# Performance work log

Measured on AMD Instinct MI355X. Metric: run time of the kernel, lower is better.

The kernel has to match this reference:

```python
import jax, jax.numpy as jnp
import numpy as np

N = 200000
E = 5000000


def _gcn_norm(edge_index, num_nodes):
    # add self-loops and compute symmetric normalization (PyG GCNConv default)
    loop = jnp.arange(num_nodes, dtype=edge_index.dtype)
    src = jnp.concatenate([edge_index[0], loop])
    dst = jnp.concatenate([edge_index[1], loop])
    ones = jnp.ones(dst.shape[0], dtype=jnp.float32)
    deg = jax.ops.segment_sum(ones, dst, num_segments=num_nodes)
    dis = jnp.where(deg > 0, jax.lax.rsqrt(deg), 0.0)
    norm = dis[src] * dis[dst]  # [E+N]
    return src, dst, norm


def _gcn_layer(x, src, dst, norm, W, b, num_nodes):
    xl = x @ W  # [N, out] dense linear (no bias, PyG default)
    msg = xl[src] * norm[:, None]  # gather + scale
    agg = jax.ops.segment_sum(msg, dst, num_segments=num_nodes)  # scatter-add
    return agg + b


def setup_inputs() -> dict:
    key = jax.random.key(0)
    ks = jax.random.split(key, 10)
    x = jax.random.normal(ks[0], (N, 12), dtype=jnp.float32)
    edge_index = jax.random.randint(ks[1], (2, E), 0, N, dtype=jnp.int64)
    def glorot(k, fi, fo):
        s = np.sqrt(6.0 / (fi + fo)).astype(np.float32)
        return jax.random.uniform(k, (fi, fo), jnp.float32, -s, s)
    return {
        "x": x,
        "edge_index": edge_index,
        "W1": glorot(ks[2], 12, 16), "b1": jnp.zeros((16,), jnp.float32),
        "W2": glorot(ks[3], 16, 8), "b2": jnp.zeros((8,), jnp.float32),
        "W3": glorot(ks[4], 8, 16), "b3": jnp.zeros((16,), jnp.float32),
        "W4": glorot(ks[5], 16, 12), "b4": jnp.zeros((12,), jnp.float32),
    }


def reference(x, edge_index, W1, b1, W2, b2, W3, b3, W4, b4):
    num_nodes = x.shape[0]
    src, dst, norm = _gcn_norm(edge_index, num_nodes)
    # Encoder
    h = jax.nn.relu(_gcn_layer(x, src, dst, norm, W1, b1, num_nodes))
    h = _gcn_layer(h, src, dst, norm, W2, b2, num_nodes)
    # Decoder
    h = jax.nn.relu(_gcn_layer(h, src, dst, norm, W3, b3, num_nodes))
    h = jax.nn.sigmoid(_gcn_layer(h, src, dst, norm, W4, b4, num_nodes))
    return h
```

## Files before the change

kernel.cpp:

```cpp
#include <hip/hip_runtime.h>
#include <hip/hip_fp16.h>
#include <math.h>


#define NPB 1024
#define MAX_NB 256
#define CAP 26496
#define BIN_CHUNK 4096
#define BIN_TH 512
#define EPT (BIN_CHUNK / BIN_TH)
#define MAXB CAP

__global__ void init_cur_kernel(int* __restrict__ bucket_cur, int NB) {
    int t = blockIdx.x * blockDim.x + threadIdx.x;
    if (t < NB) bucket_cur[t] = t * CAP;
}

__global__ __launch_bounds__(BIN_TH) void bin_kernel(const int* __restrict__ src,
                                                     const int* __restrict__ dst,
                                                     int* __restrict__ bucket_cur,
                                                     unsigned int* __restrict__ binned,
                                                     int E, int NB) {
    __shared__ int h[MAX_NB];
    __shared__ int scl[MAX_NB + 1];
    __shared__ int base[MAX_NB];
    __shared__ int sscan[256];
    __shared__ unsigned int stage[BIN_CHUNK];
    __shared__ unsigned char bkt8[BIN_CHUNK];
    int cbeg = blockIdx.x * BIN_CHUNK;
    int cend = min(cbeg + BIN_CHUNK, E);
    int chunk_n = cend - cbeg;
    int tid = threadIdx.x;

    for (int t = tid; t < NB; t += BIN_TH) h[t] = 0;
    __syncthreads();
    int myd[EPT];
#pragma unroll
    for (int j = 0; j < EPT; j++) {
        int e = cbeg + tid + j * BIN_TH;
        if (e < cend) {
            myd[j] = dst[e];
            atomicAdd(&h[myd[j] >> 10], 1);
        }
    }
    __syncthreads();
    int v = (tid < NB) ? h[tid] : 0;
    if (tid < 256) sscan[tid] = v;
    __syncthreads();
    for (int off = 1; off < 256; off <<= 1) {
        int t = (tid >= off && tid < 256) ? sscan[tid - off] : 0;
        __syncthreads();
        if (tid < 256) sscan[tid] += t;
        __syncthreads();
    }
    if (tid < NB) {
        scl[tid] = sscan[tid] - v;
        base[tid] = v ? atomicAdd(&bucket_cur[tid], v) : 0;
    }
    if (tid == 0) scl[NB] = chunk_n;
    __syncthreads();
    for (int t = tid; t < NB; t += BIN_TH) h[t] = 0;
    __syncthreads();
#pragma unroll
    for (int j = 0; j < EPT; j++) {
        int e = cbeg + tid + j * BIN_TH;
        if (e < cend) {
            int d = myd[j];
            int bkt = d >> 10;
            int pos = scl[bkt] + atomicAdd(&h[bkt], 1);
            stage[pos] = ((unsigned)src[e] << 10) | (unsigned)(d & 1023);
            bkt8[pos] = (unsigned char)bkt;
        }
    }
    __syncthreads();
    for (int k = tid; k < chunk_n; k += BIN_TH) {
        int bkt = bkt8[k];
        binned[base[bkt] + (k - scl[bkt])] = stage[k];
    }
}

__global__ __launch_bounds__(1024) void csr_bucket_t1_kernel(
    const unsigned int* __restrict__ binned,
    const int* __restrict__ bucket_cur,
    int2* __restrict__ rows, float* __restrict__ dis,
    int* __restrict__ col,
    const float* __restrict__ x, const float* __restrict__ W1,
    __half* __restrict__ xls, int N) {
    __shared__ int cnt[NPB];
    __shared__ int cur[NPB];
    __shared__ int colbuf[MAXB];
    __shared__ float sW[12 * 16];
    int b = blockIdx.x;
    int nbase = b << 10;
    int nlocal = min(NPB, N - nbase);
    int beg = b * CAP;
    int bsize = bucket_cur[b] - beg;
    int tid = threadIdx.x;

    if (tid < 192) sW[tid] = W1[tid];
    cnt[tid] = 0;
    __syncthreads();
    for (int k = tid; k < bsize; k += 1024)
        atomicAdd(&cnt[binned[beg + k] & 1023u], 1);
    __syncthreads();
    int v = cnt[tid];
    cur[tid] = v;
    __syncthreads();
    for (int off = 1; off < 1024; off <<= 1) {
        int t = (tid >= off) ? cur[tid - off] : 0;
        __syncthreads();
        cur[tid] += t;
        __syncthreads();
    }
    int excl = cur[tid] - v;
    float d = 1.0f / sqrtf((float)(v + 1));
    if (tid < nlocal) {
        rows[nbase + tid] = make_int2(beg + excl, beg + excl + v);
        dis[nbase + tid] = d;
    }
    __syncthreads();
    cur[tid] = excl;
    __syncthreads();
    if (bsize <= MAXB) {
        for (int k = tid; k < bsize; k += 1024) {
            unsigned rec = binned[beg + k];
            int pos = atomicAdd(&cur[rec & 1023u], 1);
            colbuf[pos] = (int)(rec >> 10);
        }
        __syncthreads();
        for (int k = tid; k < bsize; k += 1024) col[beg + k] = colbuf[k];
    } else {
        for (int k = tid; k < bsize; k += 1024) {
            unsigned rec = binned[beg + k];
            int pos = atomicAdd(&cur[rec & 1023u], 1);
            col[beg + pos] = (int)(rec >> 10);
        }
    }
    if (tid < nlocal) {
        int i = nbase + tid;
        float h[12];
#pragma unroll
        for (int k = 0; k < 12; k++) h[k] = x[(size_t)i * 12 + k];
        float o[16];
#pragma unroll
        for (int f = 0; f < 16; f++) {
            float acc = 0.0f;
#pragma unroll
            for (int k = 0; k < 12; k++) acc = fmaf(h[k], sW[k * 16 + f], acc);
            o[f] = acc * d;
        }
        __half2* x2 = (__half2*)xls;
#pragma unroll
        for (int c = 0; c < 2; c++) {
#pragma unroll
            for (int k = 0; k < 4; k++) {
                x2[(size_t)c * N * 4 + (size_t)i * 4 + k] =
                    __floats2half2_rn(o[c * 8 + 2 * k], o[c * 8 + 2 * k + 1]);
            }
        }
    }
}

template <int IN, int OUT, int C, int PREACT, bool SPLITIN>
__global__ __launch_bounds__(256) void transform_kernel(
    const float* __restrict__ hin0, const float* __restrict__ hin1,
    const float* __restrict__ bias_prev,
    const float* __restrict__ W, const float* __restrict__ dis,
    __half* __restrict__ xls, int N) {
    __shared__ float sW[IN * OUT];
    __shared__ float sB[IN];
    for (int t = threadIdx.x; t < IN * OUT; t += blockDim.x) sW[t] = W[t];
    if (PREACT != 0) {
        for (int t = threadIdx.x; t < IN; t += blockDim.x) sB[t] = bias_prev[t];
    }
    __syncthreads();
    int i = blockIdx.x * blockDim.x + threadIdx.x;
    if (i >= N) return;

    constexpr int CIN = SPLITIN ? IN / 2 : IN;
    float h[IN];
#pragma unroll
    for (int k = 0; k < IN; k++) {
        float v;
        if (SPLITIN)
            v = (k < CIN) ? hin0[(size_t)i * CIN + k]
                          : hin1[(size_t)i * CIN + (k - CIN)];
        else
            v = hin0[(size_t)i * IN + k];
        if (PREACT != 0) {
            v += sB[k];
            if (PREACT == 1) v = fmaxf(v, 0.0f);
        }
        h[k] = v;
    }
    float d = dis[i];
    float o[OUT];
#pragma unroll
    for (int f = 0; f < OUT; f++) {
        float acc = 0.0f;
#pragma unroll
        for (int k = 0; k < IN; k++) acc = fmaf(h[k], sW[k * OUT + f], acc);
        o[f] = acc * d;
    }
    constexpr int NCH = OUT / C;
    constexpr int P = C / 2;
    __half2* x2 = (__half2*)xls;
#pragma unroll
    for (int c = 0; c < NCH; c++) {
#pragma unroll
        for (int k = 0; k < P; k++) {
            x2[(size_t)c * N * P + (size_t)i * P + k] =
                __floats2half2_rn(o[c * C + 2 * k], o[c * C + 2 * k + 1]);
        }
    }
}

template <int P>
__device__ __forceinline__ void acc_node(const __half2* __restrict__ x2, int c,
                                         float2 (&acc)[P]) {
    __half2 t[P];
#pragma unroll
    for (int k = 0; k < P; k++) t[k] = x2[(size_t)c * P + k];
#pragma unroll
    for (int k = 0; k < P; k++) {
        float2 v = __half22float2(t[k]);
        acc[k].x += v.x;
        acc[k].y += v.y;
    }
}

template <int P>
__device__ __forceinline__ void acc_quad(const __half2* __restrict__ x2, int4 c,
                                         float2 (&acc)[P]) {
    __half2 t[4][P];
#pragma unroll
    for (int k = 0; k < P; k++) t[0][k] = x2[(size_t)c.x * P + k];
#pragma unroll
    for (int k = 0; k < P; k++) t[1][k] = x2[(size_t)c.y * P + k];
#pragma unroll
    for (int k = 0; k < P; k++) t[2][k] = x2[(size_t)c.z * P + k];
#pragma unroll
    for (int k = 0; k < P; k++) t[3][k] = x2[(size_t)c.w * P + k];
#pragma unroll
    for (int k = 0; k < P; k++) {
        float2 a0 = __half22float2(t[0][k]), a1 = __half22float2(t[1][k]);
        float2 a2 = __half22float2(t[2][k]), a3 = __half22float2(t[3][k]);
        acc[k].x += (a0.x + a1.x) + (a2.x + a3.x);
        acc[k].y += (a0.y + a1.y) + (a2.y + a3.y);
    }
}

template <int C>
__device__ __forceinline__ void gather_acc(
    int i, int p, const int2* __restrict__ rows, const int* __restrict__ col,
    const __half2* __restrict__ x2, float2 (&acc)[C / 2]) {
    constexpr int P = C / 2;
#pragma unroll
    for (int k = 0; k < P; k++) {
        if (p == 0) acc[k] = __half22float2(x2[(size_t)i * P + k]);
        else acc[k] = make_float2(0.0f, 0.0f);
    }
    int2 r = rows[i];
    int beg = r.x;
    int end = r.y;
    int nedge = end - beg;
    int pre = (4 - (beg & 3)) & 3;
    if (pre > nedge) pre = nedge;
    for (int j = p; j < pre; j += 2) acc_node<P>(x2, col[beg + j], acc);
    int abeg = beg + pre;
    int nq = (end - abeg) >> 2;
    int q = p;
    for (; q + 4 < nq; q += 6) {
        int4 ca = *reinterpret_cast<const int4*>(col + abeg + 4 * q);
        int4 cb = *reinterpret_cast<const int4*>(col + abeg + 4 * (q + 2));
        int4 cc = *reinterpret_cast<const int4*>(col + abeg + 4 * (q + 4));
        acc_quad<P>(x2, ca, acc);
        acc_quad<P>(x2, cb, acc);
        acc_quad<P>(x2, cc, acc);
    }
    for (; q < nq; q += 2) {
        int4 ca = *reinterpret_cast<const int4*>(col + abeg + 4 * q);
        acc_quad<P>(x2, ca, acc);
    }
    int tbeg = abeg + 4 * nq;
    for (int j = tbeg + p; j < end; j += 2) acc_node<P>(x2, col[j], acc);
#pragma unroll
    for (int k = 0; k < P; k++) {
        acc[k].x += __shfl_xor(acc[k].x, 1);
        acc[k].y += __shfl_xor(acc[k].y, 1);
    }
}

template <int C>
__global__ __launch_bounds__(256) void gather2_kernel(
    const int2* __restrict__ rows, const int* __restrict__ col,
    const float* __restrict__ dis, const __half* __restrict__ x0,
    const __half* __restrict__ x1, float* __restrict__ agg0,
    float* __restrict__ agg1, int N) {
    constexpr int P = C / 2;
    int grp = blockIdx.x >> 3;
    int sub = blockIdx.x & 7;
    int chunk = sub >> 2;
    int range = (grp << 2) + (sub & 3);
    int t2 = range * 256 + (int)threadIdx.x;
    int i = t2 >> 1;
    int p = t2 & 1;
    if (i >= N) return;
    const __half2* x2 = (const __half2*)(chunk ? x1 : x0);
    float* aggc = chunk ? agg1 : agg0;
    float2 acc[P];
    gather_acc<C>(i, p, rows, col, x2, acc);
    float d = dis[i];
    float2* ap = (float2*)(aggc + (size_t)i * C);
#pragma unroll
    for (int k = 0; k < P; k++) {
        if ((k & 1) == p) ap[k] = make_float2(acc[k].x * d, acc[k].y * d);
    }
}

__global__ __launch_bounds__(256) void gather_t3_kernel(
    const int2* __restrict__ rows, const int* __restrict__ col,
    const float* __restrict__ dis, const __half* __restrict__ xls,
    const float* __restrict__ b2, const float* __restrict__ W3,
    __half* __restrict__ xout, int N) {
    __shared__ float sW[8 * 16];
    __shared__ float sB[8];
    if (threadIdx.x < 128) sW[threadIdx.x] = W3[threadIdx.x];
    if (threadIdx.x < 8) sB[threadIdx.x] = b2[threadIdx.x];
    __syncthreads();
    int tid = blockIdx.x * blockDim.x + threadIdx.x;
    int i = tid >> 1;
    int p = tid & 1;
    if (i >= N) return;
    float2 acc[4];
    gather_acc<8>(i, p, rows, col, (const __half2*)xls, acc);
    float d = dis[i];
    float v[8];
#pragma unroll
    for (int k = 0; k < 4; k++) {
        v[2 * k] = acc[k].x * d + sB[2 * k];
        v[2 * k + 1] = acc[k].y * d + sB[2 * k + 1];
    }
    float o[8];
#pragma unroll
    for (int f = 0; f < 8; f++) {
        float a = 0.0f;
#pragma unroll
        for (int k = 0; k < 8; k++) a = fmaf(v[k], sW[k * 16 + p * 8 + f], a);
        o[f] = a * d;
    }
    __half2* x2o = (__half2*)xout;
#pragma unroll
    for (int k = 0; k < 4; k++) {
        x2o[(size_t)p * N * 4 + (size_t)i * 4 + k] =
            __floats2half2_rn(o[2 * k], o[2 * k + 1]);
    }
}

__global__ __launch_bounds__(256) void gather2_sig_kernel(
    const int2* __restrict__ rows, const int* __restrict__ col,
    const float* __restrict__ dis, const __half* __restrict__ x0,
    const __half* __restrict__ x1, const float* __restrict__ bias,
    float* __restrict__ out, int N) {
    int grp = blockIdx.x >> 3;
    int sub = blockIdx.x & 7;
    int chunk = sub >> 2;
    int range = (grp << 2) + (sub & 3);
    int t2 = range * 256 + (int)threadIdx.x;
    int i = t2 >> 1;
    int p = t2 & 1;
    if (i >= N) return;
    const __half2* x2 = (const __half2*)(chunk ? x1 : x0);
    int coff = chunk ? 6 : 0;
    float2 acc[3];
    gather_acc<6>(i, p, rows, col, x2, acc);
    float d = dis[i];
    float* op = out + (size_t)i * 12 + coff;
#pragma unroll
    for (int k = 0; k < 3; k++) {
        if ((k & 1) == p) {
            float vx = 1.0f / (1.0f + expf(-(acc[k].x * d + bias[coff + 2 * k])));
            float vy = 1.0f / (1.0f + expf(-(acc[k].y * d + bias[coff + 2 * k + 1])));
            *reinterpret_cast<float2*>(op + 2 * k) = make_float2(vx, vy);
        }
    }
}

static inline size_t align_up(size_t v, size_t a) { return (v + a - 1) & ~(a - 1); }

extern "C" void kernel_launch(void* const* d_in, const int* in_sizes, int n_in,
                              void* d_out, int out_size, void* d_ws, size_t ws_size,
                              hipStream_t stream) {
    const float* x  = (const float*)d_in[0];
    const int*   ei = (const int*)d_in[1];
    const float* W1 = (const float*)d_in[2];
    const float* b1 = (const float*)d_in[3];
    const float* W2 = (const float*)d_in[4];
    const float* b2 = (const float*)d_in[5];
    const float* W3 = (const float*)d_in[6];
    const float* b3 = (const float*)d_in[7];
    const float* W4 = (const float*)d_in[8];
    const float* b4 = (const float*)d_in[9];
    float* out = (float*)d_out;

    const int N = in_sizes[0] / 12;
    const int E = in_sizes[1] / 2;
    const int* src = ei;
    const int* dst = ei + E;
    const int NB = (N + NPB - 1) / NPB;

    char* ws = (char*)d_ws;
    size_t off = 0;
    int* bucket_cur = (int*)(ws + off);   off = align_up(off + (size_t)NB * 4, 256);
    int2* rows = (int2*)(ws + off);       off = align_up(off + (size_t)N * 8, 256);
    float* dis = (float*)(ws + off);      off = align_up(off + (size_t)N * 4, 256);
    unsigned int* binned = (unsigned int*)(ws + off);
    off = align_up(off + ((size_t)NB * CAP + 4096) * 4, 256);
    int* col = (int*)(ws + off);          off = align_up(off + ((size_t)NB * CAP + 4096) * 4, 256);
    __half* xls = (__half*)(ws + off);    off = align_up(off + (size_t)N * 16 * 2, 256);
    __half* xls2 = (__half*)(ws + off);   off = align_up(off + (size_t)N * 16 * 2, 256);
    float* aggA = (float*)(ws + off);     off = align_up(off + (size_t)N * 16 * 4, 256);
    (void)ws_size; (void)n_in; (void)out_size;

    const int B = 256;
    auto blocks = [&](long long n) { return (int)((n + B - 1) / B); };
    int nb2 = blocks(2LL * N);
    nb2 = (nb2 + 3) & ~3;
    const int G2 = nb2 * 2;

    init_cur_kernel<<<1, 256, 0, stream>>>(bucket_cur, NB);
    bin_kernel<<<(E + BIN_CHUNK - 1) / BIN_CHUNK, BIN_TH, 0, stream>>>(src, dst, bucket_cur, binned, E, NB);
    csr_bucket_t1_kernel<<<NB, 1024, 0, stream>>>(binned, bucket_cur, rows, dis, col,
                                                  x, W1, xls, N);

    __half* x_c0 = xls;
    __half* x_c8 = xls + (size_t)N * 8;
    __half* x_c6 = xls + (size_t)N * 6;
    __half* x2_c0 = xls2;
    __half* x2_c8 = xls2 + (size_t)N * 8;
    float* aggA0 = aggA;
    float* aggA1 = aggA + (size_t)N * 8;

    gather2_kernel<8><<<G2, B, 0, stream>>>(rows, col, dis, x_c0, x_c8, aggA0, aggA1, N);

    transform_kernel<16, 8, 8, 1, true><<<blocks(N), B, 0, stream>>>(
        aggA0, aggA1, b1, W2, dis, xls, N);

    gather_t3_kernel<<<blocks(2LL * N), B, 0, stream>>>(rows, col, dis, x_c0,
                                                        b2, W3, xls2, N);

    gather2_kernel<8><<<G2, B, 0, stream>>>(rows, col, dis, x2_c0, x2_c8, aggA0, aggA1, N);

    transform_kernel<16, 12, 6, 1, true><<<blocks(N), B, 0, stream>>>(
        aggA0, aggA1, b3, W4, dis, xls, N);

    gather2_sig_kernel<<<G2, B, 0, stream>>>(rows, col, dis, x_c0, x_c6, b4, out, N);
}
```

Measured before the change: 405.2 us.

## Degree-sort nodes within 128-node groups to balance warp work in gathers

```diff
diff --git a/kernel.cpp b/kernel.cpp
--- a/kernel.cpp
+++ b/kernel.cpp
@@ -83,7 +83,7 @@
     const unsigned int* __restrict__ binned,
     const int* __restrict__ bucket_cur,
     int2* __restrict__ rows, float* __restrict__ dis,
-    int* __restrict__ col,
+    int* __restrict__ col, int* __restrict__ perm,
     const float* __restrict__ x, const float* __restrict__ W1,
     __half* __restrict__ xls, int N) {
     __shared__ int cnt[NPB];
@@ -135,6 +135,18 @@
             int pos = atomicAdd(&cur[rec & 1023u], 1);
             col[beg + pos] = (int)(rec >> 10);
         }
+    }
+    if (tid < nlocal) {
+        int sub = tid >> 7;
+        int sbase = sub << 7;
+        int scount = min(128, nlocal - sbase);
+        int lane = tid & 127;
+        int rank = 0;
+        for (int j = 0; j < scount; j++) {
+            int dj = cnt[sbase + j];
+            rank += (dj < v) || (dj == v && j < lane);
+        }
+        perm[nbase + sbase + rank] = nbase + tid;
     }
     if (tid < nlocal) {
         int i = nbase + tid;
@@ -293,6 +305,7 @@
 
 template <int C>
 __global__ __launch_bounds__(256) void gather2_kernel(
+    const int* __restrict__ perm,
     const int2* __restrict__ rows, const int* __restrict__ col,
     const float* __restrict__ dis, const __half* __restrict__ x0,
     const __half* __restrict__ x1, float* __restrict__ agg0,
@@ -303,9 +316,10 @@
     int chunk = sub >> 2;
     int range = (grp << 2) + (sub & 3);
     int t2 = range * 256 + (int)threadIdx.x;
-    int i = t2 >> 1;
+    int slot = t2 >> 1;
     int p = t2 & 1;
-    if (i >= N) return;
+    if (slot >= N) return;
+    int i = perm[slot];
     const __half2* x2 = (const __half2*)(chunk ? x1 : x0);
     float* aggc = chunk ? agg1 : agg0;
     float2 acc[P];
@@ -319,6 +333,7 @@
 }
 
 __global__ __launch_bounds__(256) void gather_t3_kernel(
+    const int* __restrict__ perm,
     const int2* __restrict__ rows, const int* __restrict__ col,
     const float* __restrict__ dis, const __half* __restrict__ xls,
     const float* __restrict__ b2, const float* __restrict__ W3,
@@ -328,10 +343,11 @@
     if (threadIdx.x < 128) sW[threadIdx.x] = W3[threadIdx.x];
     if (threadIdx.x < 8) sB[threadIdx.x] = b2[threadIdx.x];
     __syncthreads();
-    int tid = blockIdx.x * blockDim.x + threadIdx.x;
-    int i = tid >> 1;
-    int p = tid & 1;
-    if (i >= N) return;
+    int t2 = blockIdx.x * blockDim.x + threadIdx.x;
+    int slot = t2 >> 1;
+    int p = t2 & 1;
+    if (slot >= N) return;
+    int i = perm[slot];
     float2 acc[4];
     gather_acc<8>(i, p, rows, col, (const __half2*)xls, acc);
     float d = dis[i];
@@ -358,6 +374,7 @@
 }
 
 __global__ __launch_bounds__(256) void gather2_sig_kernel(
+    const int* __restrict__ perm,
     const int2* __restrict__ rows, const int* __restrict__ col,
     const float* __restrict__ dis, const __half* __restrict__ x0,
     const __half* __restrict__ x1, const float* __restrict__ bias,
@@ -367,9 +384,10 @@
     int chunk = sub >> 2;
     int range = (grp << 2) + (sub & 3);
     int t2 = range * 256 + (int)threadIdx.x;
-    int i = t2 >> 1;
+    int slot = t2 >> 1;
     int p = t2 & 1;
-    if (i >= N) return;
+    if (slot >= N) return;
+    int i = perm[slot];
     const __half2* x2 = (const __half2*)(chunk ? x1 : x0);
     int coff = chunk ? 6 : 0;
     float2 acc[3];
@@ -414,6 +432,7 @@
     int* bucket_cur = (int*)(ws + off);   off = align_up(off + (size_t)NB * 4, 256);
     int2* rows = (int2*)(ws + off);       off = align_up(off + (size_t)N * 8, 256);
     float* dis = (float*)(ws + off);      off = align_up(off + (size_t)N * 4, 256);
+    int* perm = (int*)(ws + off);         off = align_up(off + (size_t)N * 4, 256);
     unsigned int* binned = (unsigned int*)(ws + off);
     off = align_up(off + ((size_t)NB * CAP + 4096) * 4, 256);
     int* col = (int*)(ws + off);          off = align_up(off + ((size_t)NB * CAP + 4096) * 4, 256);
@@ -431,7 +450,7 @@
     init_cur_kernel<<<1, 256, 0, stream>>>(bucket_cur, NB);
     bin_kernel<<<(E + BIN_CHUNK - 1) / BIN_CHUNK, BIN_TH, 0, stream>>>(src, dst, bucket_cur, binned, E, NB);
     csr_bucket_t1_kernel<<<NB, 1024, 0, stream>>>(binned, bucket_cur, rows, dis, col,
-                                                  x, W1, xls, N);
+                                                  perm, x, W1, xls, N);
 
     __half* x_c0 = xls;
     __half* x_c8 = xls + (size_t)N * 8;
@@ -441,18 +460,18 @@
     float* aggA0 = aggA;
     float* aggA1 = aggA + (size_t)N * 8;
 
-    gather2_kernel<8><<<G2, B, 0, stream>>>(rows, col, dis, x_c0, x_c8, aggA0, aggA1, N);
+    gather2_kernel<8><<<G2, B, 0, stream>>>(perm, rows, col, dis, x_c0, x_c8, aggA0, aggA1, N);
 
     transform_kernel<16, 8, 8, 1, true><<<blocks(N), B, 0, stream>>>(
         aggA0, aggA1, b1, W2, dis, xls, N);
 
-    gather_t3_kernel<<<blocks(2LL * N), B, 0, stream>>>(rows, col, dis, x_c0,
+    gather_t3_kernel<<<blocks(2LL * N), B, 0, stream>>>(perm, rows, col, dis, x_c0,
                                                         b2, W3, xls2, N);
 
-    gather2_kernel<8><<<G2, B, 0, stream>>>(rows, col, dis, x2_c0, x2_c8, aggA0, aggA1, N);
+    gather2_kernel<8><<<G2, B, 0, stream>>>(perm, rows, col, dis, x2_c0, x2_c8, aggA0, aggA1, N);
 
     transform_kernel<16, 12, 6, 1, true><<<blocks(N), B, 0, stream>>>(
         aggA0, aggA1, b3, W4, dis, xls, N);
 
-    gather2_sig_kernel<<<G2, B, 0, stream>>>(rows, col, dis, x_c0, x_c6, b4, out, N);
-}
+    gather2_sig_kernel<<<G2, B, 0, stream>>>(perm, rows, col, dis, x_c0, x_c6, b4, out, N);
+}
```

Measured after the change: 414.2 us. 1.02x slower.
